# Kernel tuning notes

Hardware: AMD Instinct MI355X
Metric: run time of the kernel (lower is better)

Reference implementation:

```python
import jax, jax.numpy as jnp
import numpy as np

N = 50000      # nodes
E = 500000     # edges
D = 32         # hidden_dim
ED = 16        # edge_dim
MSG_IN = 2 * D + ED
EPS = 1e-5


def setup_inputs() -> dict:
    key = jax.random.key(0)
    ks = jax.random.split(key, 16)

    def lin(k, fan_in, fan_out):
        s = 1.0 / np.sqrt(fan_in)
        return jax.random.uniform(k, (fan_in, fan_out), jnp.float32, -s, s)

    return {
        "t": jnp.zeros((), jnp.float32),
        "h": jax.random.normal(ks[0], (N, D), jnp.float32),
        "edge_attr": jax.random.normal(ks[1], (E, ED), jnp.float32),
        "Q": jax.random.normal(ks[2], (E, D, D), jnp.float32) * (1.0 / np.sqrt(D)),
        # msg_net: 2-layer MLP (Linear -> ReLU -> Linear)
        "W1": lin(ks[3], MSG_IN, D), "b1": jnp.zeros((D,), jnp.float32),
        "W2": lin(ks[4], D, D),      "b2": jnp.zeros((D,), jnp.float32),
        # dynamics_net: Linear(2D,D) -> LayerNorm -> SiLU -> Linear(D,D) -> Tanh
        "Wd1": lin(ks[5], 2 * D, D), "bd1": jnp.zeros((D,), jnp.float32),
        "ln_g": jnp.ones((D,), jnp.float32), "ln_b": jnp.zeros((D,), jnp.float32),
        "Wd2": lin(ks[6], D, D),     "bd2": jnp.zeros((D,), jnp.float32),
        "edge_index": jax.random.randint(ks[7], (2, E), 0, N, jnp.int64),
    }


def reference(t, h, edge_attr, Q, W1, b1, W2, b2, Wd1, bd1, ln_g, ln_b, Wd2, bd2, edge_index):
    row, col = edge_index[0], edge_index[1]
    # sheaf transport of source states: Q_uv @ h[col]
    h_transported = jnp.einsum('eij,ej->ei', Q, h[col])          # [E, D]
    msg_input = jnp.concatenate([h[row], h_transported, edge_attr], axis=-1)  # [E, 2D+ED]
    hidden = jax.nn.relu(msg_input @ W1 + b1)
    messages = hidden @ W2 + b2                                   # [E, D]
    agg = jax.ops.segment_sum(messages, row, num_segments=N)      # [N, D]
    x = jnp.concatenate([h, agg], axis=-1) @ Wd1 + bd1            # [N, D]
    mu = jnp.mean(x, axis=-1, keepdims=True)
    var = jnp.mean((x - mu) ** 2, axis=-1, keepdims=True)
    x = (x - mu) * jax.lax.rsqrt(var + EPS) * ln_g + ln_b
    x = jax.nn.silu(x)
    return jnp.tanh(x @ Wd2 + bd2)                                # dh/dt [N, D]
```

## Files before the change

### kernel.cpp

```cpp
#include <hip/hip_runtime.h>
#include <math.h>

#define N_NODES 50000
#define E_EDGES 500000
#define D 32
#define ED 16
#define NBLK 2048
#define NW_TOTAL (NBLK * 4)

typedef float vf4 __attribute__((ext_vector_type(4)));

struct Stage {
    vf4 q0, q1, q2, q3;
    vf4 hc;
    vf4 st;
};

__device__ __forceinline__ int2 ld_idx(const int* __restrict__ eidx, long long e) {
    int2 rc;
    rc.x = eidx[e];
    rc.y = eidx[E_EDGES + e];
    return rc;
}

__global__ __launch_bounds__(256) void edge_kernel(
    const float* __restrict__ h, const float* __restrict__ edge_attr,
    const float* __restrict__ Q, const float* __restrict__ W1,
    const float* __restrict__ b1, const float* __restrict__ W2,
    const float* __restrict__ b2, const int* __restrict__ eidx,
    float* __restrict__ agg)
{
    const int lane = threadIdx.x & 63;
    const int wib  = threadIdx.x >> 6;
    const int gwave = blockIdx.x * 4 + wib;

    const int o   = lane & 31;
    const int hh  = lane >> 5;
    const int g   = lane >> 3;
    const int sub = lane & 7;

    float w1c[40];
#pragma unroll
    for (int i = 0; i < 40; ++i) {
        const int p = hh * 40 + i;
        int f;
        if (p < 32)      f = p;
        else if (p < 64) f = 32 + ((p - 32) & 3) * 8 + ((p - 32) >> 2);
        else             f = p;
        w1c[i] = W1[f * D + o];
    }
    float w2c[16];
#pragma unroll
    for (int i = 0; i < 16; ++i) w2c[i] = W2[(hh * 16 + i) * D + o];
    const float b1o = b1[o];
    const float b2o = b2[o];

    __shared__ __align__(16) float msg_s[4][112];
    float* m = msg_s[wib];

    const long long nw = NW_TOTAL;
    long long e = gwave;
    int2 rcc = ld_idx(eidx, e);

    auto issue = [&](Stage& S, long long ee, int row, int col)
        __attribute__((always_inline)) {
        const float* qe = Q + (size_t)ee * (D * D);
        S.hc = *(const vf4*)(h + (size_t)col * D + sub * 4);
        if (lane < 12) {
            const float* gsrc = (lane < 8)
                ? (h + (size_t)row * D + lane * 4)
                : (edge_attr + (size_t)ee * ED + (lane - 8) * 4);
            S.st = *(const vf4*)gsrc;
        }
        S.q0 = __builtin_nontemporal_load((const vf4*)(qe + 0 * 256 + lane * 4));
        S.q1 = __builtin_nontemporal_load((const vf4*)(qe + 1 * 256 + lane * 4));
        S.q2 = __builtin_nontemporal_load((const vf4*)(qe + 2 * 256 + lane * 4));
        S.q3 = __builtin_nontemporal_load((const vf4*)(qe + 3 * 256 + lane * 4));
    };

    auto compute = [&](const Stage& S, int row)
        __attribute__((always_inline)) {
        if (lane < 12) {
            float* dst = (lane < 8) ? (m + lane * 4) : (m + 64 + (lane - 8) * 4);
            *(vf4*)dst = S.st;
        }
        float a0 = S.q0.x * S.hc.x + S.q0.y * S.hc.y + S.q0.z * S.hc.z + S.q0.w * S.hc.w;
        float a1 = S.q1.x * S.hc.x + S.q1.y * S.hc.y + S.q1.z * S.hc.z + S.q1.w * S.hc.w;
        float a2 = S.q2.x * S.hc.x + S.q2.y * S.hc.y + S.q2.z * S.hc.z + S.q2.w * S.hc.w;
        float a3 = S.q3.x * S.hc.x + S.q3.y * S.hc.y + S.q3.z * S.hc.z + S.q3.w * S.hc.w;
#pragma unroll
        for (int mm = 1; mm <= 4; mm <<= 1) {
            a0 += __shfl_xor(a0, mm);
            a1 += __shfl_xor(a1, mm);
            a2 += __shfl_xor(a2, mm);
            a3 += __shfl_xor(a3, mm);
        }
        if (sub == 0) {
            vf4 t; t.x = a0; t.y = a1; t.z = a2; t.w = a3;
            *(vf4*)(m + 32 + g * 4) = t;
        }
        float s = 0.f;
        const vf4* mv = (const vf4*)(m + hh * 40);
#pragma unroll
        for (int i4 = 0; i4 < 10; ++i4) {
            const vf4 v = mv[i4];
            s = fmaf(v.x, w1c[4 * i4 + 0], s);
            s = fmaf(v.y, w1c[4 * i4 + 1], s);
            s = fmaf(v.z, w1c[4 * i4 + 2], s);
            s = fmaf(v.w, w1c[4 * i4 + 3], s);
        }
        s += __shfl_xor(s, 32);
        s = fmaxf(s + b1o, 0.f);
        if (lane < 32) m[80 + o] = s;
        float t = 0.f;
        const vf4* hv = (const vf4*)(m + 80 + hh * 16);
#pragma unroll
        for (int i4 = 0; i4 < 4; ++i4) {
            const vf4 v = hv[i4];
            t = fmaf(v.x, w2c[4 * i4 + 0], t);
            t = fmaf(v.y, w2c[4 * i4 + 1], t);
            t = fmaf(v.z, w2c[4 * i4 + 2], t);
            t = fmaf(v.w, w2c[4 * i4 + 3], t);
        }
        t += __shfl_xor(t, 32);
        t += b2o;
        if (lane < 32) atomicAdd(&agg[(size_t)row * D + o], t);
    };

    const long long e1 = e + nw;
    int2 rcn = make_int2(0, 0);
    if (e1 < E_EDGES) rcn = ld_idx(eidx, e1);

    Stage A, B;
    issue(A, e, rcc.x, rcc.y);
    if (e1 < E_EDGES) issue(B, e1, rcn.x, rcn.y);

    while (true) {
        {
            const long long e2 = e + 2 * nw;
            int2 rc2 = make_int2(0, 0);
            if (e2 < E_EDGES) rc2 = ld_idx(eidx, e2);
            compute(A, rcc.x);
            if (e2 < E_EDGES) issue(A, e2, rc2.x, rc2.y);
            rcc = rcn; rcn = rc2;
            e += nw;
            if (e >= E_EDGES) break;
        }
        {
            const long long e2 = e + 2 * nw;
            int2 rc2 = make_int2(0, 0);
            if (e2 < E_EDGES) rc2 = ld_idx(eidx, e2);
            compute(B, rcc.x);
            if (e2 < E_EDGES) issue(B, e2, rc2.x, rc2.y);
            rcc = rcn; rcn = rc2;
            e += nw;
            if (e >= E_EDGES) break;
        }
    }
}

__global__ __launch_bounds__(256) void node_kernel(
    const float* __restrict__ h, const float* __restrict__ agg,
    const float* __restrict__ Wd1, const float* __restrict__ bd1,
    const float* __restrict__ ln_g, const float* __restrict__ ln_b,
    const float* __restrict__ Wd2, const float* __restrict__ bd2,
    float* __restrict__ out)
{
    __shared__ float sWd1[64 * 32];
    __shared__ float sWd2[32 * 32];
    __shared__ float xbuf[4][64];

    for (int i = threadIdx.x; i < 64 * 32; i += 256) sWd1[i] = Wd1[i];
    for (int i = threadIdx.x; i < 32 * 32; i += 256) sWd2[i] = Wd2[i];
    __syncthreads();

    const int tid  = blockIdx.x * 256 + threadIdx.x;
    const int n    = tid >> 5;
    const int o    = tid & 31;
    const int wib  = threadIdx.x >> 6;
    const int lane = threadIdx.x & 63;
    if (n >= N_NODES) return;

    const float* hn = h   + (size_t)n * D;
    const float* an = agg + (size_t)n * D;

    float x = bd1[o];
#pragma unroll
    for (int k4 = 0; k4 < 8; ++k4) {
        const float4 hv = *reinterpret_cast<const float4*>(hn + k4 * 4);
        x = fmaf(hv.x, sWd1[(k4 * 4 + 0) * 32 + o], x);
        x = fmaf(hv.y, sWd1[(k4 * 4 + 1) * 32 + o], x);
        x = fmaf(hv.z, sWd1[(k4 * 4 + 2) * 32 + o], x);
        x = fmaf(hv.w, sWd1[(k4 * 4 + 3) * 32 + o], x);
    }
#pragma unroll
    for (int k4 = 0; k4 < 8; ++k4) {
        const float4 av = *reinterpret_cast<const float4*>(an + k4 * 4);
        x = fmaf(av.x, sWd1[(32 + k4 * 4 + 0) * 32 + o], x);
        x = fmaf(av.y, sWd1[(32 + k4 * 4 + 1) * 32 + o], x);
        x = fmaf(av.z, sWd1[(32 + k4 * 4 + 2) * 32 + o], x);
        x = fmaf(av.w, sWd1[(32 + k4 * 4 + 3) * 32 + o], x);
    }

    float mu = x;
#pragma unroll
    for (int mm = 1; mm <= 16; mm <<= 1) mu += __shfl_xor(mu, mm);
    mu *= (1.0f / 32.0f);
    const float dx = x - mu;
    float var = dx * dx;
#pragma unroll
    for (int mm = 1; mm <= 16; mm <<= 1) var += __shfl_xor(var, mm);
    var *= (1.0f / 32.0f);
    float xs = dx * rsqrtf(var + 1e-5f);
    xs = xs * ln_g[o] + ln_b[o];
    xs = xs / (1.0f + __expf(-xs));

    xbuf[wib][lane] = xs;

    float y = bd2[o];
    const float* xb = &xbuf[wib][lane & 32];
#pragma unroll
    for (int k4 = 0; k4 < 8; ++k4) {
        const float4 xv = *reinterpret_cast<const float4*>(xb + k4 * 4);
        y = fmaf(xv.x, sWd2[(k4 * 4 + 0) * 32 + o], y);
        y = fmaf(xv.y, sWd2[(k4 * 4 + 1) * 32 + o], y);
        y = fmaf(xv.z, sWd2[(k4 * 4 + 2) * 32 + o], y);
        y = fmaf(xv.w, sWd2[(k4 * 4 + 3) * 32 + o], y);
    }
    out[(size_t)n * D + o] = tanhf(y);
}

extern "C" void kernel_launch(void* const* d_in, const int* in_sizes, int n_in,
                              void* d_out, int out_size, void* d_ws, size_t ws_size,
                              hipStream_t stream) {
    const float* h         = (const float*)d_in[1];
    const float* edge_attr = (const float*)d_in[2];
    const float* Q         = (const float*)d_in[3];
    const float* W1        = (const float*)d_in[4];
    const float* b1        = (const float*)d_in[5];
    const float* W2        = (const float*)d_in[6];
    const float* b2        = (const float*)d_in[7];
    const float* Wd1       = (const float*)d_in[8];
    const float* bd1       = (const float*)d_in[9];
    const float* ln_g      = (const float*)d_in[10];
    const float* ln_b      = (const float*)d_in[11];
    const float* Wd2       = (const float*)d_in[12];
    const float* bd2       = (const float*)d_in[13];
    const int*   eidx      = (const int*)d_in[14];

    float* agg = (float*)d_ws;
    hipMemsetAsync(agg, 0, (size_t)N_NODES * D * sizeof(float), stream);

    edge_kernel<<<NBLK, 256, 0, stream>>>(h, edge_attr, Q, W1, b1, W2, b2, eidx, agg);
    node_kernel<<<(N_NODES * D + 255) / 256, 256, 0, stream>>>(
        h, agg, Wd1, bd1, ln_g, ln_b, Wd2, bd2, (float*)d_out);
}
```

Measured before the change: 446.7 us.

## Stream Q tiles into LDS via async global_load_lds double buffering

```diff
diff --git a/kernel.cpp b/kernel.cpp
--- a/kernel.cpp
+++ b/kernel.cpp
@@ -10,11 +10,12 @@
 
 typedef float vf4 __attribute__((ext_vector_type(4)));
 
-struct Stage {
-    vf4 q0, q1, q2, q3;
-    vf4 hc;
-    vf4 st;
-};
+__device__ __forceinline__ void dma16(const float* g, float* l) {
+    __builtin_amdgcn_global_load_lds(
+        (const __attribute__((address_space(1))) void*)(g),
+        (__attribute__((address_space(3))) void*)(l),
+        16 , 0, 0);
+}
 
 __device__ __forceinline__ int2 ld_idx(const int* __restrict__ eidx, long long e) {
     int2 rc;
@@ -23,7 +24,7 @@
     return rc;
 }
 
-__global__ __launch_bounds__(256) void edge_kernel(
+__global__ __launch_bounds__(256, 4) void edge_kernel(
     const float* __restrict__ h, const float* __restrict__ edge_attr,
     const float* __restrict__ Q, const float* __restrict__ W1,
     const float* __restrict__ b1, const float* __restrict__ W2,
@@ -55,39 +56,41 @@
     const float b1o = b1[o];
     const float b2o = b2[o];
 
+    __shared__ __align__(16) float qlds[4][2][1024];
     __shared__ __align__(16) float msg_s[4][112];
-    float* m = msg_s[wib];
-
-    const long long nw = NW_TOTAL;
-    long long e = gwave;
-    int2 rcc = ld_idx(eidx, e);
-
-    auto issue = [&](Stage& S, long long ee, int row, int col)
+    float* m  = msg_s[wib];
+    float* qb0 = &qlds[wib][0][0];
+    float* qb1 = &qlds[wib][1][0];
+
+    auto issue = [&](float* qbuf, long long ee, int row, int col, vf4& hcS, vf4& stS)
         __attribute__((always_inline)) {
         const float* qe = Q + (size_t)ee * (D * D);
-        S.hc = *(const vf4*)(h + (size_t)col * D + sub * 4);
+#pragma unroll
+        for (int k = 0; k < 4; ++k)
+            dma16(qe + k * 256 + lane * 4, qbuf + k * 256);
+        hcS = *(const vf4*)(h + (size_t)col * D + sub * 4);
         if (lane < 12) {
             const float* gsrc = (lane < 8)
                 ? (h + (size_t)row * D + lane * 4)
                 : (edge_attr + (size_t)ee * ED + (lane - 8) * 4);
-            S.st = *(const vf4*)gsrc;
-        }
-        S.q0 = __builtin_nontemporal_load((const vf4*)(qe + 0 * 256 + lane * 4));
-        S.q1 = __builtin_nontemporal_load((const vf4*)(qe + 1 * 256 + lane * 4));
-        S.q2 = __builtin_nontemporal_load((const vf4*)(qe + 2 * 256 + lane * 4));
-        S.q3 = __builtin_nontemporal_load((const vf4*)(qe + 3 * 256 + lane * 4));
+            stS = *(const vf4*)gsrc;
+        }
     };
 
-    auto compute = [&](const Stage& S, int row)
+    auto compute = [&](const float* qbuf, const vf4 hcS, const vf4 stS, int row)
         __attribute__((always_inline)) {
         if (lane < 12) {
             float* dst = (lane < 8) ? (m + lane * 4) : (m + 64 + (lane - 8) * 4);
-            *(vf4*)dst = S.st;
-        }
-        float a0 = S.q0.x * S.hc.x + S.q0.y * S.hc.y + S.q0.z * S.hc.z + S.q0.w * S.hc.w;
-        float a1 = S.q1.x * S.hc.x + S.q1.y * S.hc.y + S.q1.z * S.hc.z + S.q1.w * S.hc.w;
-        float a2 = S.q2.x * S.hc.x + S.q2.y * S.hc.y + S.q2.z * S.hc.z + S.q2.w * S.hc.w;
-        float a3 = S.q3.x * S.hc.x + S.q3.y * S.hc.y + S.q3.z * S.hc.z + S.q3.w * S.hc.w;
+            *(vf4*)dst = stS;
+        }
+        const vf4 q0 = *(const vf4*)(qbuf + 0 * 256 + lane * 4);
+        const vf4 q1 = *(const vf4*)(qbuf + 1 * 256 + lane * 4);
+        const vf4 q2 = *(const vf4*)(qbuf + 2 * 256 + lane * 4);
+        const vf4 q3 = *(const vf4*)(qbuf + 3 * 256 + lane * 4);
+        float a0 = q0.x * hcS.x + q0.y * hcS.y + q0.z * hcS.z + q0.w * hcS.w;
+        float a1 = q1.x * hcS.x + q1.y * hcS.y + q1.z * hcS.z + q1.w * hcS.w;
+        float a2 = q2.x * hcS.x + q2.y * hcS.y + q2.z * hcS.z + q2.w * hcS.w;
+        float a3 = q3.x * hcS.x + q3.y * hcS.y + q3.z * hcS.z + q3.w * hcS.w;
 #pragma unroll
         for (int mm = 1; mm <= 4; mm <<= 1) {
             a0 += __shfl_xor(a0, mm);
@@ -127,35 +130,43 @@
         if (lane < 32) atomicAdd(&agg[(size_t)row * D + o], t);
     };
 
-    const long long e1 = e + nw;
-    int2 rcn = make_int2(0, 0);
-    if (e1 < E_EDGES) rcn = ld_idx(eidx, e1);
-
-    Stage A, B;
-    issue(A, e, rcc.x, rcc.y);
-    if (e1 < E_EDGES) issue(B, e1, rcn.x, rcn.y);
+    const long long nw = NW_TOTAL;
+    long long e = gwave;
+    if (e >= E_EDGES) return;
+
+    vf4 hcA, stA, hcB, stB;
+    int2 rc_cur = ld_idx(eidx, e);
+    issue(qb0, e, rc_cur.x, rc_cur.y, hcA, stA);
+
+    long long en = e + nw;
+    bool haveN = en < E_EDGES;
+    int2 rc_nxt;
+    if (haveN) rc_nxt = ld_idx(eidx, en);
 
     while (true) {
-        {
-            const long long e2 = e + 2 * nw;
-            int2 rc2 = make_int2(0, 0);
-            if (e2 < E_EDGES) rc2 = ld_idx(eidx, e2);
-            compute(A, rcc.x);
-            if (e2 < E_EDGES) issue(A, e2, rc2.x, rc2.y);
-            rcc = rcn; rcn = rc2;
-            e += nw;
-            if (e >= E_EDGES) break;
-        }
-        {
-            const long long e2 = e + 2 * nw;
-            int2 rc2 = make_int2(0, 0);
-            if (e2 < E_EDGES) rc2 = ld_idx(eidx, e2);
-            compute(B, rcc.x);
-            if (e2 < E_EDGES) issue(B, e2, rc2.x, rc2.y);
-            rcc = rcn; rcn = rc2;
-            e += nw;
-            if (e >= E_EDGES) break;
-        }
+        if (haveN) {
+            issue(qb1, en, rc_nxt.x, rc_nxt.y, hcB, stB);
+            asm volatile("s_waitcnt vmcnt(6)" ::: "memory");
+        } else {
+            asm volatile("s_waitcnt vmcnt(0)" ::: "memory");
+        }
+        compute(qb0, hcA, stA, rc_cur.x);
+        if (!haveN) break;
+        e = en; rc_cur = rc_nxt;
+        en = e + nw; haveN = en < E_EDGES;
+        if (haveN) rc_nxt = ld_idx(eidx, en);
+
+        if (haveN) {
+            issue(qb0, en, rc_nxt.x, rc_nxt.y, hcA, stA);
+            asm volatile("s_waitcnt vmcnt(6)" ::: "memory");
+        } else {
+            asm volatile("s_waitcnt vmcnt(0)" ::: "memory");
+        }
+        compute(qb1, hcB, stB, rc_cur.x);
+        if (!haveN) break;
+        e = en; rc_cur = rc_nxt;
+        en = e + nw; haveN = en < E_EDGES;
+        if (haveN) rc_nxt = ld_idx(eidx, en);
     }
 }
 
```

Measured after the change: 479.1 us. 1.07x slower.
